# Optimization experiments

Hardware: AMD Instinct MI355X
Metric: run time of the kernel (lower is better)

Reference implementation:

```python
import jax, jax.numpy as jnp
import numpy as np

EPS = 1e-12  # torch F.normalize eps
NUM_HEADS = 4
DT = 0.25
NUM_STEPS = 4


def _l2norm(x, axis=-1):
    n = jnp.sqrt(jnp.sum(x * x, axis=axis, keepdims=True))
    return x / jnp.maximum(n, EPS)


def setup_inputs() -> dict:
    key = jax.random.key(0)
    k0, k1, k2, k3, k4 = jax.random.split(key, 5)
    B, T, D = 4, 2048, 256
    z = jax.random.normal(k0, (B, T, D), dtype=jnp.float32)
    omega = jax.random.normal(k1, (1, 1, D), dtype=jnp.float32) * 0.1
    Wqk = jax.random.normal(k2, (2 * D, D), dtype=jnp.float32) * (1.0 / np.sqrt(D))
    Wout = jax.random.normal(k3, (D, D), dtype=jnp.float32) * (1.0 / np.sqrt(D))
    bout = jax.random.normal(k4, (D,), dtype=jnp.float32) * 0.01
    return {"z": z, "omega": omega, "Wqk": Wqk, "Wout": Wout, "bout": bout}


def _kuramoto(x, omega, Wqk, Wout, bout):
    # x: [B, T, D]
    B, T, D = x.shape
    hd = D // NUM_HEADS
    qk = x @ Wqk.T  # [B, T, 2D]
    q, k = jnp.split(qk, 2, axis=-1)
    q = _l2norm(q.reshape(B, T, NUM_HEADS, hd))  # cosine-normalized per head
    k = _l2norm(k.reshape(B, T, NUM_HEADS, hd))
    # coupling: [B, H, T, T] cosine similarity
    coupling = jnp.einsum("bqhd,bkhd->bhqk", q, k)
    # sin nonlinearity replaces softmax
    force = jnp.einsum("bhqk,bkhd->bqhd", jnp.sin(coupling), k).reshape(B, T, D)
    return omega + force @ Wout.T + bout


def reference(z, omega, Wqk, Wout, bout):
    def f(x):
        return _kuramoto(x, omega, Wqk, Wout, bout)

    x = z
    for _ in range(NUM_STEPS):
        x = _l2norm(x)
        k1 = f(x)
        k2 = f(x + DT / 2 * k1)
        k3 = f(x + DT / 2 * k2)
        k4 = f(x + DT * k3)
        x = x + DT / 6 * (k1 + 2 * k2 + 2 * k3 + k4)
    return _l2norm(x)
```

## Files before the change

kernel.cpp:

```cpp
#include <hip/hip_runtime.h>
#include <cmath>

#define NB 4
#define TT 2048
#define DD 256
#define NH 4
#define BT (NB*TT)

static constexpr float DT_ = 0.25f;

typedef _Float16 f16x8 __attribute__((ext_vector_type(8)));
typedef _Float16 f16x4 __attribute__((ext_vector_type(4)));
typedef float    f32x4 __attribute__((ext_vector_type(4)));
typedef float    f32x16 __attribute__((ext_vector_type(16)));

static constexpr size_t HSZ = (size_t)NB * NH * TT * 64;
static constexpr size_t FSZ = (size_t)BT * 256;

__device__ __forceinline__ void gload16(const void* g, void* l) {
    __builtin_amdgcn_global_load_lds(
        (const __attribute__((address_space(1))) void*)g,
        (__attribute__((address_space(3))) void*)l,
        16, 0, 0);
}

__global__ __launch_bounds__(256)
void split_weights(const float* __restrict__ Wqk, const float* __restrict__ Wout,
                   _Float16* __restrict__ WqkH, _Float16* __restrict__ WqkL,
                   _Float16* __restrict__ WoutH, _Float16* __restrict__ WoutL)
{
    const int idx = blockIdx.x * 256 + threadIdx.x;
    const float4 v = (idx < 32768) ? ((const float4*)Wqk)[idx]
                                   : ((const float4*)Wout)[idx - 32768];
    f16x4 h, l;
    h[0]=(_Float16)v.x; l[0]=(_Float16)(v.x-(float)h[0]);
    h[1]=(_Float16)v.y; l[1]=(_Float16)(v.y-(float)h[1]);
    h[2]=(_Float16)v.z; l[2]=(_Float16)(v.z-(float)h[2]);
    h[3]=(_Float16)v.w; l[3]=(_Float16)(v.w-(float)h[3]);
    if (idx < 32768) { ((f16x4*)WqkH)[idx] = h; ((f16x4*)WqkL)[idx] = l; }
    else { ((f16x4*)WoutH)[idx-32768] = h; ((f16x4*)WoutL)[idx-32768] = l; }
}

__global__ __launch_bounds__(256)
void comb_weights(const float* __restrict__ Wqk, const float* __restrict__ Wout,
                  const float* __restrict__ omega, const float* __restrict__ bout,
                  _Float16* __restrict__ WcombH, _Float16* __restrict__ WcombL,
                  float* __restrict__ qkob)
{
    __shared__ float qrow[256];
    __shared__ float pr[256];
    const int n = blockIdx.x;
    const int k = threadIdx.x;
    qrow[k] = Wqk[n * 256 + k];
    __syncthreads();
    float s = 0.f;
    for (int m = 0; m < 256; ++m) s = fmaf(qrow[m], Wout[m * 256 + k], s);
    const _Float16 h = (_Float16)s;
    WcombH[n * 256 + k] = h;
    WcombL[n * 256 + k] = (_Float16)(s - (float)h);
    pr[k] = (omega[k] + bout[k]) * qrow[k];
    __syncthreads();
    if (k == 0) {
        float t = 0.f;
        for (int i = 0; i < 256; ++i) t += pr[i];
        qkob[n] = t;
    }
}

__global__ __launch_bounds__(256)
void l2norm_rows(const float* __restrict__ src, float* __restrict__ dst,
                 _Float16* __restrict__ dstH, _Float16* __restrict__ dstL) {
    const int wave = threadIdx.x >> 6;
    const int lane = threadIdx.x & 63;
    const size_t row = (size_t)blockIdx.x * 4 + wave;
    float4 v = ((const float4*)(src + row * DD))[lane];
    float ss = v.x*v.x + v.y*v.y + v.z*v.z + v.w*v.w;
    #pragma unroll
    for (int off = 32; off; off >>= 1) ss += __shfl_xor(ss, off, 64);
    const float inv = 1.0f / fmaxf(sqrtf(ss), 1e-12f);
    v.x *= inv; v.y *= inv; v.z *= inv; v.w *= inv;
    ((float4*)(dst + row * DD))[lane] = v;
    if (dstH != nullptr) {
        f16x4 h, l;
        h[0]=(_Float16)v.x; l[0]=(_Float16)(v.x-(float)h[0]);
        h[1]=(_Float16)v.y; l[1]=(_Float16)(v.y-(float)h[1]);
        h[2]=(_Float16)v.z; l[2]=(_Float16)(v.z-(float)h[2]);
        h[3]=(_Float16)v.w; l[3]=(_Float16)(v.w-(float)h[3]);
        ((f16x4*)(dstH + row * DD))[lane] = h;
        ((f16x4*)(dstL + row * DD))[lane] = l;
    }
}

__global__ __launch_bounds__(256, 2)
void gemm_mfma(const _Float16* __restrict__ AH, const _Float16* __restrict__ AL,
               const _Float16* __restrict__ BH, const _Float16* __restrict__ BL,
               const float* __restrict__ Fp, float* __restrict__ FaccP,
               float* __restrict__ qkx, const float* __restrict__ qkob,
               const float* __restrict__ omega, const float* __restrict__ bout,
               const float* __restrict__ xin, float* __restrict__ xout,
               _Float16* __restrict__ Qhi, _Float16* __restrict__ Qlo,
               _Float16* __restrict__ Khi, _Float16* __restrict__ Klo,
               _Float16* __restrict__ KtrH,
               int mode, float cc, int faccm)
{
    __shared__ _Float16 Ah[128 * 64];
    __shared__ _Float16 Al[128 * 64];
    __shared__ _Float16 Bh[64 * 64];
    __shared__ _Float16 Bl[64 * 64];
    const int m0 = blockIdx.x * 128, n0 = blockIdx.y * 64;
    const int t  = threadIdx.x;
    const int w  = t >> 6;
    const int l  = t & 63;
    const int lr = l & 15;
    const int lq = l >> 4;
    const int m7 = lr & 7;
    const int rr = l >> 3;
    const int lc  = l & 7;
    const int cg  = (lc ^ rr) * 8;
    const int swd = (lc ^ rr) * 8;
    const bool yzero = (blockIdx.y == 0);

    f32x4 acc[2][4];
    #pragma unroll
    for (int s = 0; s < 2; ++s)
        #pragma unroll
        for (int nt = 0; nt < 4; ++nt) acc[s][nt] = (f32x4){0.f,0.f,0.f,0.f};

#define GSTAGE_A(K0) do { \
        _Pragma("unroll") \
        for (int a = 0; a < 4; ++a) { \
            const int rg = 8*w + 32*a; \
            gload16(AH + (size_t)(m0 + rg + rr) * 256 + (K0) + cg, &Ah[rg * 64]); \
            gload16(AL + (size_t)(m0 + rg + rr) * 256 + (K0) + cg, &Al[rg * 64]); \
        } \
    } while (0)

#define GSTAGE_B(K0) do { \
        _Pragma("unroll") \
        for (int a = 0; a < 2; ++a) { \
            const int rg = 8*w + 32*a; \
            gload16(BH + (size_t)(n0 + rg + rr) * 256 + (K0) + cg, &Bh[rg * 64]); \
            gload16(BL + (size_t)(n0 + rg + rr) * 256 + (K0) + cg, &Bl[rg * 64]); \
        } \
    } while (0)

#define FSTAGE(K0) do { \
        _Pragma("unroll") \
        for (int a = 0; a < 4; ++a) { \
            const int row = 8*w + 32*a + rr; \
            const size_t go = (size_t)(m0 + row) * 256 + (K0) + lc * 8; \
            float sv[8]; \
            { const float4 a0 = *(const float4*)(Fp + go); \
              const float4 a1 = *(const float4*)(Fp + go + 4); \
              sv[0]=a0.x; sv[1]=a0.y; sv[2]=a0.z; sv[3]=a0.w; \
              sv[4]=a1.x; sv[5]=a1.y; sv[6]=a1.z; sv[7]=a1.w; } \
            _Pragma("unroll") \
            for (int p = 1; p < 3; ++p) { \
                const float4 a0 = *(const float4*)(Fp + (size_t)p*FSZ + go); \
                const float4 a1 = *(const float4*)(Fp + (size_t)p*FSZ + go + 4); \
                sv[0]+=a0.x; sv[1]+=a0.y; sv[2]+=a0.z; sv[3]+=a0.w; \
                sv[4]+=a1.x; sv[5]+=a1.y; sv[6]+=a1.z; sv[7]+=a1.w; } \
            if (faccm == 3) { \
                const float4 f0 = *(const float4*)(FaccP + go); \
                const float4 f1 = *(const float4*)(FaccP + go + 4); \
                sv[0]+=f0.x; sv[1]+=f0.y; sv[2]+=f0.z; sv[3]+=f0.w; \
                sv[4]+=f1.x; sv[5]+=f1.y; sv[6]+=f1.z; sv[7]+=f1.w; \
            } else if (yzero) { \
                if (faccm == 1) { \
                    *(float4*)(FaccP + go)     = make_float4(sv[0], sv[1], sv[2], sv[3]); \
                    *(float4*)(FaccP + go + 4) = make_float4(sv[4], sv[5], sv[6], sv[7]); \
                } else { \
                    float4 f0 = *(const float4*)(FaccP + go); \
                    float4 f1 = *(const float4*)(FaccP + go + 4); \
                    f0.x += 2.f*sv[0]; f0.y += 2.f*sv[1]; f0.z += 2.f*sv[2]; f0.w += 2.f*sv[3]; \
                    f1.x += 2.f*sv[4]; f1.y += 2.f*sv[5]; f1.z += 2.f*sv[6]; f1.w += 2.f*sv[7]; \
                    *(float4*)(FaccP + go)     = f0; \
                    *(float4*)(FaccP + go + 4) = f1; \
                } \
            } \
            f16x8 hv, lv; \
            _Pragma("unroll") \
            for (int e = 0; e < 8; ++e) { \
                hv[e] = (_Float16)sv[e]; \
                lv[e] = (_Float16)(sv[e] - (float)hv[e]); } \
            *(f16x8*)&Ah[row * 64 + swd] = hv; \
            *(f16x8*)&Al[row * 64 + swd] = lv; \
        } \
    } while (0)

    if (mode == 0) GSTAGE_A(0); else FSTAGE(0);
    GSTAGE_B(0);
    asm volatile("s_waitcnt vmcnt(0) lgkmcnt(0)" ::: "memory");
    __builtin_amdgcn_s_barrier();
    asm volatile("" ::: "memory");

    for (int kc = 0; kc < 4; ++kc) {
        f16x8 ah[2][2], al[2][2], bh[2][4], bl[2][4];
        #pragma unroll
        for (int c = 0; c < 2; ++c) {
            const int xo = (((4*c + lq) ^ m7) << 4);
            #pragma unroll
            for (int s = 0; s < 2; ++s) {
                ah[c][s] = *(const f16x8*)((const char*)Ah + (32*w + 16*s + lr) * 128 + xo);
                al[c][s] = *(const f16x8*)((const char*)Al + (32*w + 16*s + lr) * 128 + xo);
            }
            #pragma unroll
            for (int nt = 0; nt < 4; ++nt) {
                bh[c][nt] = *(const f16x8*)((const char*)Bh + (16*nt + lr) * 128 + xo);
                bl[c][nt] = *(const f16x8*)((const char*)Bl + (16*nt + lr) * 128 + xo);
            }
        }
        asm volatile("s_waitcnt lgkmcnt(0)" ::: "memory");
        __builtin_amdgcn_s_barrier();
        asm volatile("" ::: "memory");
        if (kc < 3) {
            GSTAGE_B((kc + 1) * 64);
            if (mode == 0) GSTAGE_A((kc + 1) * 64); else FSTAGE((kc + 1) * 64);
        }
        #pragma unroll
        for (int c = 0; c < 2; ++c)
            #pragma unroll
            for (int s = 0; s < 2; ++s)
                #pragma unroll
                for (int nt = 0; nt < 4; ++nt) {
                    acc[s][nt] = __builtin_amdgcn_mfma_f32_16x16x32_f16(ah[c][s], bh[c][nt], acc[s][nt], 0, 0, 0);
                    acc[s][nt] = __builtin_amdgcn_mfma_f32_16x16x32_f16(ah[c][s], bl[c][nt], acc[s][nt], 0, 0, 0);
                    acc[s][nt] = __builtin_amdgcn_mfma_f32_16x16x32_f16(al[c][s], bh[c][nt], acc[s][nt], 0, 0, 0);
                }
        if (kc < 3) asm volatile("s_waitcnt vmcnt(0) lgkmcnt(0)" ::: "memory");
        __builtin_amdgcn_s_barrier();
        asm volatile("" ::: "memory");
    }
#undef GSTAGE_A
#undef GSTAGE_B
#undef FSTAGE

    if (mode == 2) {
        #pragma unroll
        for (int s = 0; s < 2; ++s) {
            const int row0 = m0 + 32*w + 16*s + 4*lq;
            #pragma unroll
            for (int nt = 0; nt < 4; ++nt) {
                const int col = n0 + 16*nt + lr;
                const float ob = omega[col] + bout[col];
                #pragma unroll
                for (int r = 0; r < 4; ++r) {
                    const size_t off = (size_t)(row0 + r) * 256 + col;
                    xout[off] = xin[off] + (DT_ / 6.0f) * acc[s][nt][r] + DT_ * ob;
                }
            }
        }
    } else {
        float val[2][4][4];
        #pragma unroll
        for (int s = 0; s < 2; ++s) {
            const int row0 = m0 + 32*w + 16*s + 4*lq;
            #pragma unroll
            for (int nt = 0; nt < 4; ++nt) {
                const int col = n0 + 16*nt + lr;
                #pragma unroll
                for (int r = 0; r < 4; ++r) {
                    const size_t qo = (size_t)(row0 + r) * 512 + col;
                    if (mode == 0) {
                        val[s][nt][r] = acc[s][nt][r];
                        qkx[qo] = acc[s][nt][r];
                    } else {
                        val[s][nt][r] = qkx[qo] + cc * (acc[s][nt][r] + qkob[col]);
                    }
                }
            }
        }
        float ss[2][4];
        #pragma unroll
        for (int s = 0; s < 2; ++s)
            #pragma unroll
            for (int r = 0; r < 4; ++r) {
                float v = 0.f;
                #pragma unroll
                for (int nt = 0; nt < 4; ++nt) v += val[s][nt][r] * val[s][nt][r];
                ss[s][r] = v;
            }
        #pragma unroll
        for (int off = 1; off < 16; off <<= 1)
            #pragma unroll
            for (int s = 0; s < 2; ++s)
                #pragma unroll
                for (int r = 0; r < 4; ++r)
                    ss[s][r] += __shfl_xor(ss[s][r], off, 64);
        const int  b    = m0 >> 11;
        const int  h    = (n0 >> 6) & 3;
        const bool is_k = (n0 >= 256);
        const size_t bhi = (size_t)b * NH + h;
        _Float16* dhi = (is_k ? Khi : Qhi) + bhi * (size_t)TT * 64;
        _Float16* dlo = (is_k ? Klo : Qlo) + bhi * (size_t)TT * 64;
        const int mloc = m0 & (TT - 1);
        _Float16* Pt = Ah;
        #pragma unroll
        for (int s = 0; s < 2; ++s) {
            const int r0 = 32*w + 16*s + 4*lq;
            float inv[4];
            #pragma unroll
            for (int r = 0; r < 4; ++r) inv[r] = 1.0f / fmaxf(sqrtf(ss[s][r]), 1e-12f);
            #pragma unroll
            for (int nt = 0; nt < 4; ++nt) {
                const int d = 16*nt + lr;
                f16x4 hv, lv;
                #pragma unroll
                for (int r = 0; r < 4; ++r) {
                    const float v2 = val[s][nt][r] * inv[r];
                    hv[r] = (_Float16)v2;
                    lv[r] = (_Float16)(v2 - (float)hv[r]);
                    dhi[(size_t)(mloc + r0 + r) * 64 + d] = hv[r];
                    dlo[(size_t)(mloc + r0 + r) * 64 + d] = lv[r];
                }
                if (is_k) {
                    *(f16x4*)((char*)Pt + d * 256 + ((r0 * 2) ^ ((d & 7) << 4))) = hv;
                }
            }
        }
        if (is_k) {
            __syncthreads();
            const size_t kb = bhi * (size_t)64 * TT + mloc;
            #pragma unroll
            for (int p = 0; p < 4; ++p) {
                const int d   = (t >> 4) + 16 * p;
                const int g   = t & 15;
                const int win = g >> 3, gw = g & 7;
                const int Ga  = 16*win + 4*(gw >> 1) + (gw & 1);
                const int Gb  = Ga + 2;
                f16x4 va = *(const f16x4*)((const char*)Pt + d * 256 + ((8*Ga) ^ ((d & 7) << 4)));
                f16x4 vb = *(const f16x4*)((const char*)Pt + d * 256 + ((8*Gb) ^ ((d & 7) << 4)));
                f16x8 v;
                #pragma unroll
                for (int e = 0; e < 4; ++e) { v[e] = va[e]; v[4 + e] = vb[e]; }
                *(f16x8*)(KtrH + kb + (size_t)d * TT + 8*g) = v;
            }
        }
    }
}

__global__ __launch_bounds__(256, 3)
void kuramoto_attn(const _Float16* __restrict__ Qhi, const _Float16* __restrict__ Qlo,
                   const _Float16* __restrict__ Khi, const _Float16* __restrict__ Klo,
                   const _Float16* __restrict__ KtrH,
                   float* __restrict__ Fp)
{
    __shared__ _Float16 KjH[64 * 64];
    __shared__ _Float16 KjL[64 * 64];
    __shared__ _Float16 KdH[64 * 64];
    const int bh = blockIdx.x;
    const int b  = bh >> 2, h = bh & 3;
    const size_t base  = (size_t)bh * TT * 64;
    const size_t tbase = (size_t)bh * 64 * TT;
    const int t0 = blockIdx.y * 11;
    const int tn = (blockIdx.y == 2) ? 10 : 11;
    float* Fout = Fp + (size_t)blockIdx.y * FSZ;
    const int t = threadIdx.x;
    const int w = t >> 6;
    const int l = t & 63;
    const int il = l & 31;
    const int h5 = l >> 5;
    const int i0 = blockIdx.z * 128 + w * 32;
    const int s7 = il & 7;
    const int rr = l >> 3;
    const int cg = ((l & 7) ^ rr) * 8;

    f16x8 qh[4], ql[4];
    #pragma unroll
    for (int kc = 0; kc < 4; ++kc) {
        const size_t qoff = base + (size_t)(i0 + il) * 64 + 16*kc + 8*h5;
        qh[kc] = *(const f16x8*)(Qhi + qoff);
        ql[kc] = *(const f16x8*)(Qlo + qoff);
    }

    f32x16 Fac[2];
    #pragma unroll
    for (int db = 0; db < 2; ++db)
        #pragma unroll
        for (int r = 0; r < 16; ++r) Fac[db][r] = 0.f;

    for (int tt = 0; tt < tn; ++tt) {
        const int j0 = (t0 + tt) * 64;
        __syncthreads();
        gload16(Khi + base + (size_t)(j0 + 8*w + rr) * 64 + cg,       &KjH[(8*w) * 64]);
        gload16(Khi + base + (size_t)(j0 + 8*w + rr + 32) * 64 + cg,  &KjH[(8*w + 32) * 64]);
        gload16(Klo + base + (size_t)(j0 + 8*w + rr) * 64 + cg,       &KjL[(8*w) * 64]);
        gload16(Klo + base + (size_t)(j0 + 8*w + rr + 32) * 64 + cg,  &KjL[(8*w + 32) * 64]);
        gload16(KtrH + tbase + (size_t)(8*w + rr) * TT + j0 + cg,     &KdH[(8*w) * 64]);
        gload16(KtrH + tbase + (size_t)(8*w + rr + 32) * TT + j0 + cg,&KdH[(8*w + 32) * 64]);
        asm volatile("s_waitcnt vmcnt(0)" ::: "memory");
        __syncthreads();

        f16x8 ph[2][2];
        #pragma unroll
        for (int jb = 0; jb < 2; ++jb) {
            f32x16 sA, sB;
            #pragma unroll
            for (int r = 0; r < 16; ++r) { sA[r] = 0.f; sB[r] = 0.f; }
            const int rowb = (32*jb + il) * 128;
            __builtin_amdgcn_s_setprio(1);
            #pragma unroll
            for (int kc = 0; kc < 4; ++kc) {
                const int ch = (((2*kc + h5) ^ s7) << 4);
                f16x8 khA = *(const f16x8*)((const char*)KjH + rowb + ch);
                f16x8 klA = *(const f16x8*)((const char*)KjL + rowb + ch);
                sA = __builtin_amdgcn_mfma_f32_32x32x16_f16(khA, qh[kc], sA, 0, 0, 0);
                sB = __builtin_amdgcn_mfma_f32_32x32x16_f16(klA, qh[kc], sB, 0, 0, 0);
                sB = __builtin_amdgcn_mfma_f32_32x32x16_f16(khA, ql[kc], sB, 0, 0, 0);
            }
            __builtin_amdgcn_s_setprio(0);
            f16x8 v0, v1;
            #pragma unroll
            for (int e = 0; e < 8; ++e) {
                v0[e] = (_Float16)__sinf(sA[e] + sB[e]);
                v1[e] = (_Float16)__sinf(sA[8 + e] + sB[8 + e]);
            }
            ph[jb][0] = v0;
            ph[jb][1] = v1;
        }

        #pragma unroll
        for (int db = 0; db < 2; ++db) {
            const int rowd = (il + 32*db) * 128;
            __builtin_amdgcn_s_setprio(1);
            #pragma unroll
            for (int cp = 0; cp < 4; ++cp) {
                f16x8 kf = *(const f16x8*)((const char*)KdH + rowd + (((2*cp + h5) ^ s7) << 4));
                Fac[db] = __builtin_amdgcn_mfma_f32_32x32x16_f16(ph[cp >> 1][cp & 1], kf, Fac[db], 0, 0, 0);
            }
            __builtin_amdgcn_s_setprio(0);
        }
    }

    #pragma unroll
    for (int db = 0; db < 2; ++db)
        #pragma unroll
        for (int r = 0; r < 16; ++r) {
            const int irow = (r & 3) + 8 * (r >> 2) + 4 * h5;
            Fout[((size_t)b * TT + i0 + irow) * 256 + h * 64 + il + 32 * db] = Fac[db][r];
        }
}

extern "C" void kernel_launch(void* const* d_in, const int* in_sizes, int n_in,
                              void* d_out, int out_size, void* d_ws, size_t ws_size,
                              hipStream_t stream) {
    const float* z     = (const float*)d_in[0];
    const float* omega = (const float*)d_in[1];
    const float* Wqk   = (const float*)d_in[2];
    const float* Wout  = (const float*)d_in[3];
    const float* bout  = (const float*)d_in[4];

    float* x    = (float*)d_ws;
    float* Facc = x + FSZ;
    float* Fp   = Facc + FSZ;
    float* qkx  = Fp + 3 * FSZ;
    float* qkob = qkx + (size_t)BT * 512;
    _Float16* xsH  = (_Float16*)(qkob + 512);
    _Float16* xsL  = xsH  + FSZ;
    _Float16* Qhi  = xsL  + FSZ;
    _Float16* Qlo  = Qhi  + HSZ;
    _Float16* Khi  = Qlo  + HSZ;
    _Float16* Klo  = Khi  + HSZ;
    _Float16* KtrH = Klo  + HSZ;
    _Float16* WqkH = KtrH + HSZ;
    _Float16* WqkL = WqkH + (size_t)512 * 256;
    _Float16* WoutH= WqkL + (size_t)512 * 256;
    _Float16* WoutL= WoutH + (size_t)256 * 256;
    _Float16* WcombH = WoutL + (size_t)256 * 256;
    _Float16* WcombL = WcombH + (size_t)512 * 256;

    split_weights<<<192, 256, 0, stream>>>(Wqk, Wout, WqkH, WqkL, WoutH, WoutL);
    comb_weights<<<512, 256, 0, stream>>>(Wqk, Wout, omega, bout, WcombH, WcombL, qkob);

    for (int step = 0; step < 4; ++step) {
        l2norm_rows<<<BT / 4, 256, 0, stream>>>(step == 0 ? z : x, x, xsH, xsL);
        gemm_mfma<<<dim3(BT / 128, 8), 256, 0, stream>>>(
            xsH, xsL, WqkH, WqkL, nullptr, nullptr, qkx, nullptr,
            nullptr, nullptr, nullptr, nullptr,
            Qhi, Qlo, Khi, Klo, KtrH, 0, 0.f, 0);
        kuramoto_attn<<<dim3(NB * NH, 3, TT / 128), 256, 0, stream>>>(
            Qhi, Qlo, Khi, Klo, KtrH, Fp);
        for (int s = 1; s <= 3; ++s) {
            const float cs = (s == 3) ? 0.25f : 0.125f;
            gemm_mfma<<<dim3(BT / 128, 8), 256, 0, stream>>>(
                nullptr, nullptr, WcombH, WcombL, Fp, Facc, qkx, qkob,
                nullptr, nullptr, nullptr, nullptr,
                Qhi, Qlo, Khi, Klo, KtrH, 1, cs, (s == 1) ? 1 : 2);
            kuramoto_attn<<<dim3(NB * NH, 3, TT / 128), 256, 0, stream>>>(
                Qhi, Qlo, Khi, Klo, KtrH, Fp);
        }
        gemm_mfma<<<dim3(BT / 128, 4), 256, 0, stream>>>(
            nullptr, nullptr, WoutH, WoutL, Fp, Facc, nullptr, nullptr,
            omega, bout, x, x,
            nullptr, nullptr, nullptr, nullptr, nullptr, 2, 0.f, 3);
    }
    l2norm_rows<<<BT / 4, 256, 0, stream>>>(x, (float*)d_out, nullptr, nullptr);
}
```

Before: 1.184 ms.

## Store K in MFMA-fragment-ordered layout and read directly from global, dropping LDS staging

Result: slower. 1.362 ms (+15.0%).

```diff
diff --git a/kernel.cpp b/kernel.cpp
--- a/kernel.cpp
+++ b/kernel.cpp
@@ -99,8 +99,8 @@
                const float* __restrict__ omega, const float* __restrict__ bout,
                const float* __restrict__ xin, float* __restrict__ xout,
                _Float16* __restrict__ Qhi, _Float16* __restrict__ Qlo,
-               _Float16* __restrict__ Khi, _Float16* __restrict__ Klo,
-               _Float16* __restrict__ KtrH,
+               _Float16* __restrict__ KChi, _Float16* __restrict__ KClo,
+               _Float16* __restrict__ KD,
                int mode, float cc, int faccm)
 {
     __shared__ _Float16 Ah[128 * 64];
@@ -291,8 +291,8 @@
         const int  h    = (n0 >> 6) & 3;
         const bool is_k = (n0 >= 256);
         const size_t bhi = (size_t)b * NH + h;
-        _Float16* dhi = (is_k ? Khi : Qhi) + bhi * (size_t)TT * 64;
-        _Float16* dlo = (is_k ? Klo : Qlo) + bhi * (size_t)TT * 64;
+        _Float16* dhi = is_k ? nullptr : (Qhi + bhi * (size_t)TT * 64);
+        _Float16* dlo = is_k ? nullptr : (Qlo + bhi * (size_t)TT * 64);
         const int mloc = m0 & (TT - 1);
         _Float16* Pt = Ah;
         #pragma unroll
@@ -310,8 +310,16 @@
                     const float v2 = val[s][nt][r] * inv[r];
                     hv[r] = (_Float16)v2;
                     lv[r] = (_Float16)(v2 - (float)hv[r]);
-                    dhi[(size_t)(mloc + r0 + r) * 64 + d] = hv[r];
-                    dlo[(size_t)(mloc + r0 + r) * 64 + d] = lv[r];
+                    if (!is_k) {
+                        dhi[(size_t)(mloc + r0 + r) * 64 + d] = hv[r];
+                        dlo[(size_t)(mloc + r0 + r) * 64 + d] = lv[r];
+                    } else {
+                        const int j = mloc + r0 + r;
+                        const size_t ka = ((size_t)(bhi * 32 + (j >> 6)) * 8 + (d >> 3)) * 512
+                                          + (j & 63) * 8 + (d & 7);
+                        KChi[ka] = hv[r];
+                        KClo[ka] = lv[r];
+                    }
                 }
                 if (is_k) {
                     *(f16x4*)((char*)Pt + d * 256 + ((r0 * 2) ^ ((d & 7) << 4))) = hv;
@@ -320,7 +328,6 @@
         }
         if (is_k) {
             __syncthreads();
-            const size_t kb = bhi * (size_t)64 * TT + mloc;
             #pragma unroll
             for (int p = 0; p < 4; ++p) {
                 const int d   = (t >> 4) + 16 * p;
@@ -333,7 +340,8 @@
                 f16x8 v;
                 #pragma unroll
                 for (int e = 0; e < 4; ++e) { v[e] = va[e]; v[4 + e] = vb[e]; }
-                *(f16x8*)(KtrH + kb + (size_t)d * TT + 8*g) = v;
+                const size_t da = ((size_t)(bhi * 32 + (mloc >> 6) + win) * 8 + gw) * 512 + d * 8;
+                *(f16x8*)(KD + da) = v;
             }
         }
     }
@@ -341,17 +349,14 @@
 
 __global__ __launch_bounds__(256, 3)
 void kuramoto_attn(const _Float16* __restrict__ Qhi, const _Float16* __restrict__ Qlo,
-                   const _Float16* __restrict__ Khi, const _Float16* __restrict__ Klo,
-                   const _Float16* __restrict__ KtrH,
+                   const _Float16* __restrict__ KChi, const _Float16* __restrict__ KClo,
+                   const _Float16* __restrict__ KD,
                    float* __restrict__ Fp)
 {
-    __shared__ _Float16 KjH[64 * 64];
-    __shared__ _Float16 KjL[64 * 64];
-    __shared__ _Float16 KdH[64 * 64];
     const int bh = blockIdx.x;
     const int b  = bh >> 2, h = bh & 3;
-    const size_t base  = (size_t)bh * TT * 64;
-    const size_t tbase = (size_t)bh * 64 * TT;
+    const size_t qbase  = (size_t)bh * TT * 64;
+    const size_t kcbase = (size_t)bh * 32 * 4096;
     const int t0 = blockIdx.y * 11;
     const int tn = (blockIdx.y == 2) ? 10 : 11;
     float* Fout = Fp + (size_t)blockIdx.y * FSZ;
@@ -361,14 +366,11 @@
     const int il = l & 31;
     const int h5 = l >> 5;
     const int i0 = blockIdx.z * 128 + w * 32;
-    const int s7 = il & 7;
-    const int rr = l >> 3;
-    const int cg = ((l & 7) ^ rr) * 8;
 
     f16x8 qh[4], ql[4];
     #pragma unroll
     for (int kc = 0; kc < 4; ++kc) {
-        const size_t qoff = base + (size_t)(i0 + il) * 64 + 16*kc + 8*h5;
+        const size_t qoff = qbase + (size_t)(i0 + il) * 64 + 16*kc + 8*h5;
         qh[kc] = *(const f16x8*)(Qhi + qoff);
         ql[kc] = *(const f16x8*)(Qlo + qoff);
     }
@@ -380,16 +382,10 @@
         for (int r = 0; r < 16; ++r) Fac[db][r] = 0.f;
 
     for (int tt = 0; tt < tn; ++tt) {
-        const int j0 = (t0 + tt) * 64;
-        __syncthreads();
-        gload16(Khi + base + (size_t)(j0 + 8*w + rr) * 64 + cg,       &KjH[(8*w) * 64]);
-        gload16(Khi + base + (size_t)(j0 + 8*w + rr + 32) * 64 + cg,  &KjH[(8*w + 32) * 64]);
-        gload16(Klo + base + (size_t)(j0 + 8*w + rr) * 64 + cg,       &KjL[(8*w) * 64]);
-        gload16(Klo + base + (size_t)(j0 + 8*w + rr + 32) * 64 + cg,  &KjL[(8*w + 32) * 64]);
-        gload16(KtrH + tbase + (size_t)(8*w + rr) * TT + j0 + cg,     &KdH[(8*w) * 64]);
-        gload16(KtrH + tbase + (size_t)(8*w + rr + 32) * TT + j0 + cg,&KdH[(8*w + 32) * 64]);
-        asm volatile("s_waitcnt vmcnt(0)" ::: "memory");
-        __syncthreads();
+        const size_t tb = kcbase + (size_t)(t0 + tt) * 4096;
+        const _Float16* pH = KChi + tb;
+        const _Float16* pL = KClo + tb;
+        const _Float16* pD = KD + tb;
 
         f16x8 ph[2][2];
         #pragma unroll
@@ -397,13 +393,13 @@
             f32x16 sA, sB;
             #pragma unroll
             for (int r = 0; r < 16; ++r) { sA[r] = 0.f; sB[r] = 0.f; }
-            const int rowb = (32*jb + il) * 128;
+            const int ro = (32*jb + il) * 8;
             __builtin_amdgcn_s_setprio(1);
             #pragma unroll
             for (int kc = 0; kc < 4; ++kc) {
-                const int ch = (((2*kc + h5) ^ s7) << 4);
-                f16x8 khA = *(const f16x8*)((const char*)KjH + rowb + ch);
-                f16x8 klA = *(const f16x8*)((const char*)KjL + rowb + ch);
+                const int co = (2*kc + h5) * 512;
+                f16x8 khA = *(const f16x8*)(pH + co + ro);
+                f16x8 klA = *(const f16x8*)(pL + co + ro);
                 sA = __builtin_amdgcn_mfma_f32_32x32x16_f16(khA, qh[kc], sA, 0, 0, 0);
                 sB = __builtin_amdgcn_mfma_f32_32x32x16_f16(klA, qh[kc], sB, 0, 0, 0);
                 sB = __builtin_amdgcn_mfma_f32_32x32x16_f16(khA, ql[kc], sB, 0, 0, 0);
@@ -421,11 +417,11 @@
 
         #pragma unroll
         for (int db = 0; db < 2; ++db) {
-            const int rowd = (il + 32*db) * 128;
+            const int dro = (il + 32*db) * 8;
             __builtin_amdgcn_s_setprio(1);
             #pragma unroll
             for (int cp = 0; cp < 4; ++cp) {
-                f16x8 kf = *(const f16x8*)((const char*)KdH + rowd + (((2*cp + h5) ^ s7) << 4));
+                f16x8 kf = *(const f16x8*)(pD + (2*cp + h5) * 512 + dro);
                 Fac[db] = __builtin_amdgcn_mfma_f32_32x32x16_f16(ph[cp >> 1][cp & 1], kf, Fac[db], 0, 0, 0);
             }
             __builtin_amdgcn_s_setprio(0);
@@ -459,10 +455,10 @@
     _Float16* xsL  = xsH  + FSZ;
     _Float16* Qhi  = xsL  + FSZ;
     _Float16* Qlo  = Qhi  + HSZ;
-    _Float16* Khi  = Qlo  + HSZ;
-    _Float16* Klo  = Khi  + HSZ;
-    _Float16* KtrH = Klo  + HSZ;
-    _Float16* WqkH = KtrH + HSZ;
+    _Float16* KChi = Qlo  + HSZ;
+    _Float16* KClo = KChi + HSZ;
+    _Float16* KD   = KClo + HSZ;
+    _Float16* WqkH = KD   + HSZ;
     _Float16* WqkL = WqkH + (size_t)512 * 256;
     _Float16* WoutH= WqkL + (size_t)512 * 256;
     _Float16* WoutL= WoutH + (size_t)256 * 256;
@@ -477,17 +473,17 @@
         gemm_mfma<<<dim3(BT / 128, 8), 256, 0, stream>>>(
             xsH, xsL, WqkH, WqkL, nullptr, nullptr, qkx, nullptr,
             nullptr, nullptr, nullptr, nullptr,
-            Qhi, Qlo, Khi, Klo, KtrH, 0, 0.f, 0);
+            Qhi, Qlo, KChi, KClo, KD, 0, 0.f, 0);
         kuramoto_attn<<<dim3(NB * NH, 3, TT / 128), 256, 0, stream>>>(
-            Qhi, Qlo, Khi, Klo, KtrH, Fp);
+            Qhi, Qlo, KChi, KClo, KD, Fp);
         for (int s = 1; s <= 3; ++s) {
             const float cs = (s == 3) ? 0.25f : 0.125f;
             gemm_mfma<<<dim3(BT / 128, 8), 256, 0, stream>>>(
                 nullptr, nullptr, WcombH, WcombL, Fp, Facc, qkx, qkob,
                 nullptr, nullptr, nullptr, nullptr,
-                Qhi, Qlo, Khi, Klo, KtrH, 1, cs, (s == 1) ? 1 : 2);
+                Qhi, Qlo, KChi, KClo, KD, 1, cs, (s == 1) ? 1 : 2);
             kuramoto_attn<<<dim3(NB * NH, 3, TT / 128), 256, 0, stream>>>(
-                Qhi, Qlo, Khi, Klo, KtrH, Fp);
+                Qhi, Qlo, KChi, KClo, KD, Fp);
         }
         gemm_mfma<<<dim3(BT / 128, 4), 256, 0, stream>>>(
             nullptr, nullptr, WoutH, WoutL, Fp, Facc, nullptr, nullptr,
```
